# Performance work log

Hardware: AMD Instinct MI355X
Metric: run time of the kernel (lower is better)

Reference implementation:

```python
import jax, jax.numpy as jnp
import numpy as np

LN_EPS = 1e-5

def _layernorm(x, gamma, beta):
    mu = jnp.mean(x, axis=-1, keepdims=True)
    var = jnp.mean(jnp.square(x - mu), axis=-1, keepdims=True)
    return (x - mu) * jax.lax.rsqrt(var + LN_EPS) * gamma + beta


def setup_inputs() -> dict:
    key = jax.random.key(0)
    k1, k2 = jax.random.split(key)
    B, T, E = 8, 4096, 1024
    half = E // 2
    kernel = 15
    x = jax.random.normal(k1, (B, T, E), dtype=jnp.float32)
    weight = jax.random.normal(k2, (half, kernel), dtype=jnp.float32) * 0.02
    gamma = jnp.ones((half,), dtype=jnp.float32)
    beta = jnp.zeros((half,), dtype=jnp.float32)
    return {"x": x, "weight": weight, "gamma": gamma, "beta": beta}


def reference(x, weight, gamma, beta):
    # x: [B, T, E]; split into residual and gate halves along channels
    res, gate = jnp.split(x, 2, axis=-1)          # each [B, T, C], C = E//2
    gate = _layernorm(gate, gamma, beta)
    n = gate.shape[1]
    gate = jnp.transpose(gate, (0, 2, 1))         # [B, C, T]
    gate_f = jnp.fft.rfft(gate, n=n, axis=-1)     # [B, C, n//2+1] complex
    w_f = jnp.fft.rfft(weight, n=n, axis=-1)      # [C, n//2+1] complex
    # (gr*wr + gi*wi) + i(gi*wr - gr*wi) == gate_f * conj(w_f)
    prod = gate_f * jnp.conj(w_f)
    gate = jnp.fft.irfft(prod, n=n, axis=-1)      # [B, C, T]
    gate = jnp.transpose(gate, (0, 2, 1))         # [B, T, C]
    # act is Identity
    return gate * res
```

## Files before the change

kernel.cpp:

```cpp
#include <hip/hip_runtime.h>

#define T_DIM 4096
#define C_DIM 512
#define E_DIM 1024
#define KW 15
#define LN_EPS 1e-5f

#define TB 32
#define RT (TB + KW - 1)
#define NW 8

__global__ __launch_bounds__(512) void fgu_fused_kernel(
    const float* __restrict__ x,
    const float* __restrict__ w,
    const float* __restrict__ gamma,
    const float* __restrict__ beta,
    float* __restrict__ out)
{
    __shared__ float psum[RT][NW];
    __shared__ float pssq[RT][NW];
    __shared__ float smu[RT];
    __shared__ float srs[RT];

    const int c    = threadIdx.x;
    const int lane = c & 63;
    const int wv   = c >> 6;
    const int tile = blockIdx.x;
    const int b    = tile / (T_DIM / TB);
    const int t0   = (tile - b * (T_DIM / TB)) * TB;

    const float* xb = x + (size_t)b * T_DIM * E_DIM;

    float g[RT];
    #pragma unroll
    for (int k = 0; k < RT; ++k) {
        const int tt = (t0 + k) & (T_DIM - 1);
        g[k] = xb[(size_t)tt * E_DIM + C_DIM + c];
        float s  = g[k];
        float ss = g[k] * g[k];
        #pragma unroll
        for (int off = 32; off; off >>= 1) {
            s  += __shfl_xor(s, off);
            ss += __shfl_xor(ss, off);
        }
        if (lane == 0) { psum[k][wv] = s; pssq[k][wv] = ss; }
    }
    __syncthreads();

    if (c < RT) {
        float s = 0.0f, ss = 0.0f;
        #pragma unroll
        for (int i = 0; i < NW; ++i) { s += psum[c][i]; ss += pssq[c][i]; }
        const float mu  = s * (1.0f / (float)C_DIM);
        const float var = ss * (1.0f / (float)C_DIM) - mu * mu;
        smu[c] = mu;
        srs[c] = rsqrtf(var + LN_EPS);
    }
    __syncthreads();

    const float gm = gamma[c];
    const float bt = beta[c];
    #pragma unroll
    for (int k = 0; k < RT; ++k)
        g[k] = (g[k] - smu[k]) * srs[k] * gm + bt;

    float wreg[KW];
    const float* wc = w + c * KW;
    #pragma unroll
    for (int j = 0; j < KW; ++j) wreg[j] = wc[j];

    const float* rb = xb + (size_t)t0 * E_DIM + c;
    float*       ob = out + ((size_t)b * T_DIM + t0) * C_DIM + c;
    #pragma unroll
    for (int i = 0; i < TB; ++i) {
        float acc = 0.0f;
        #pragma unroll
        for (int j = 0; j < KW; ++j)
            acc = fmaf(g[i + j], wreg[j], acc);
        ob[(size_t)i * C_DIM] = rb[(size_t)i * E_DIM] * acc;
    }
}

extern "C" void kernel_launch(void* const* d_in, const int* in_sizes, int n_in,
                              void* d_out, int out_size, void* d_ws, size_t ws_size,
                              hipStream_t stream) {
    const float* x      = (const float*)d_in[0];
    const float* weight = (const float*)d_in[1];
    const float* gamma  = (const float*)d_in[2];
    const float* beta   = (const float*)d_in[3];
    float* out = (float*)d_out;

    const int nblocks = 8 * (T_DIM / TB);
    fgu_fused_kernel<<<nblocks, 512, 0, stream>>>(x, weight, gamma, beta, out);
}
```

Measured before the change: 274.9 us.

## Stage gate rows in LDS with float4 loads, fold gamma/beta into weights, halve tile

Each wave now loads a full gate row with float4 loads, computes the layernorm statistics per row in one wave, and stages the row in shared memory. This replaces the per-thread scalar loads and the second reduction-and-barrier pass. A small prep kernel folds gamma into the conv weights and beta times the weight sum into a bias, so normalisation becomes a single FMA. The time tile drops from 32 to 16, which shrinks register pressure but raises the halo re-read overhead and adds a second launch.

```diff
diff --git a/kernel.cpp b/kernel.cpp
--- a/kernel.cpp
+++ b/kernel.cpp
@@ -6,77 +6,100 @@
 #define KW 15
 #define LN_EPS 1e-5f
 
-#define TB 32
+#define TB 16
 #define RT (TB + KW - 1)
 #define NW 8
 
-__global__ __launch_bounds__(512) void fgu_fused_kernel(
-    const float* __restrict__ x,
+__global__ __launch_bounds__(512) void fgu_prep_kernel(
     const float* __restrict__ w,
     const float* __restrict__ gamma,
     const float* __restrict__ beta,
+    float* __restrict__ wpad)
+{
+    const int c = threadIdx.x;
+    const float gm = gamma[c];
+    const float bt = beta[c];
+    float s = 0.0f;
+    float* o = wpad + c * 16;
+    #pragma unroll
+    for (int j = 0; j < KW; ++j) {
+        const float wj = w[c * KW + j];
+        s += wj;
+        o[j] = gm * wj;
+    }
+    o[KW] = bt * s;
+}
+
+__global__ __launch_bounds__(512) void fgu_fused_kernel(
+    const float* __restrict__ x,
+    const float* __restrict__ wpad,
     float* __restrict__ out)
 {
-    __shared__ float psum[RT][NW];
-    __shared__ float pssq[RT][NW];
-    __shared__ float smu[RT];
-    __shared__ float srs[RT];
+    __shared__ float  tile[RT][C_DIM];
+    __shared__ float2 srn[RT];
 
-    const int c    = threadIdx.x;
-    const int lane = c & 63;
-    const int wv   = c >> 6;
-    const int tile = blockIdx.x;
-    const int b    = tile / (T_DIM / TB);
-    const int t0   = (tile - b * (T_DIM / TB)) * TB;
+    const int tid  = threadIdx.x;
+    const int lane = tid & 63;
+    const int wv   = tid >> 6;
+    const int b    = blockIdx.x >> 8;
+    const int t0   = (blockIdx.x & 255) * TB;
 
     const float* xb = x + (size_t)b * T_DIM * E_DIM;
 
-    float g[RT];
-    #pragma unroll
-    for (int k = 0; k < RT; ++k) {
+    for (int k = wv; k < RT; k += NW) {
         const int tt = (t0 + k) & (T_DIM - 1);
-        g[k] = xb[(size_t)tt * E_DIM + C_DIM + c];
-        float s  = g[k];
-        float ss = g[k] * g[k];
+        const float* gp = xb + (size_t)tt * E_DIM + C_DIM;
+        const float4 a  = *(const float4*)(gp + lane * 4);
+        const float4 b4 = *(const float4*)(gp + 256 + lane * 4);
+
+        float s  = a.x + a.y + a.z + a.w + b4.x + b4.y + b4.z + b4.w;
+        float ss = a.x*a.x + a.y*a.y + a.z*a.z + a.w*a.w
+                 + b4.x*b4.x + b4.y*b4.y + b4.z*b4.z + b4.w*b4.w;
         #pragma unroll
         for (int off = 32; off; off >>= 1) {
             s  += __shfl_xor(s, off);
             ss += __shfl_xor(ss, off);
         }
-        if (lane == 0) { psum[k][wv] = s; pssq[k][wv] = ss; }
+
+        *(float4*)&tile[k][lane * 4]       = a;
+        *(float4*)&tile[k][256 + lane * 4] = b4;
+
+        if (lane == 0) {
+            const float mu  = s * (1.0f / (float)C_DIM);
+            const float var = ss * (1.0f / (float)C_DIM) - mu * mu;
+            const float rs  = rsqrtf(var + LN_EPS);
+            srn[k] = make_float2(rs, -mu * rs);
+        }
     }
     __syncthreads();
 
-    if (c < RT) {
-        float s = 0.0f, ss = 0.0f;
-        #pragma unroll
-        for (int i = 0; i < NW; ++i) { s += psum[c][i]; ss += pssq[c][i]; }
-        const float mu  = s * (1.0f / (float)C_DIM);
-        const float var = ss * (1.0f / (float)C_DIM) - mu * mu;
-        smu[c] = mu;
-        srs[c] = rsqrtf(var + LN_EPS);
+    const int c = tid;
+
+    float z[RT];
+    #pragma unroll
+    for (int k = 0; k < RT; ++k) {
+        const float2 p = srn[k];
+        z[k] = fmaf(tile[k][c], p.x, p.y);
     }
-    __syncthreads();
 
-    const float gm = gamma[c];
-    const float bt = beta[c];
-    #pragma unroll
-    for (int k = 0; k < RT; ++k)
-        g[k] = (g[k] - smu[k]) * srs[k] * gm + bt;
-
-    float wreg[KW];
-    const float* wc = w + c * KW;
-    #pragma unroll
-    for (int j = 0; j < KW; ++j) wreg[j] = wc[j];
+    float wr[16];
+    {
+        const float4* wp = (const float4*)(wpad + c * 16);
+        const float4 w0 = wp[0], w1 = wp[1], w2 = wp[2], w3 = wp[3];
+        wr[0]=w0.x;  wr[1]=w0.y;  wr[2]=w0.z;  wr[3]=w0.w;
+        wr[4]=w1.x;  wr[5]=w1.y;  wr[6]=w1.z;  wr[7]=w1.w;
+        wr[8]=w2.x;  wr[9]=w2.y;  wr[10]=w2.z; wr[11]=w2.w;
+        wr[12]=w3.x; wr[13]=w3.y; wr[14]=w3.z; wr[15]=w3.w;
+    }
 
     const float* rb = xb + (size_t)t0 * E_DIM + c;
     float*       ob = out + ((size_t)b * T_DIM + t0) * C_DIM + c;
     #pragma unroll
     for (int i = 0; i < TB; ++i) {
-        float acc = 0.0f;
+        float acc = wr[KW];
         #pragma unroll
         for (int j = 0; j < KW; ++j)
-            acc = fmaf(g[i + j], wreg[j], acc);
+            acc = fmaf(z[i + j], wr[j], acc);
         ob[(size_t)i * C_DIM] = rb[(size_t)i * E_DIM] * acc;
     }
 }
@@ -88,8 +111,11 @@
     const float* weight = (const float*)d_in[1];
     const float* gamma  = (const float*)d_in[2];
     const float* beta   = (const float*)d_in[3];
-    float* out = (float*)d_out;
+    float* out  = (float*)d_out;
+    float* wpad = (float*)d_ws;
+
+    fgu_prep_kernel<<<1, 512, 0, stream>>>(weight, gamma, beta, wpad);
 
     const int nblocks = 8 * (T_DIM / TB);
-    fgu_fused_kernel<<<nblocks, 512, 0, stream>>>(x, weight, gamma, beta, out);
+    fgu_fused_kernel<<<nblocks, 512, 0, stream>>>(x, wpad, out);
 }
```

New measurement: 230.3 us. -16.2%, faster.
